# Performance work log

Measured on AMD Instinct MI355X. Metric: run time of the kernel, lower is better.

## Reference

```python
import jax, jax.numpy as jnp
import numpy as np

B, S, HID, NH, KCLIP = 2, 1500, 1024, 16, 64
HD = HID // NH  # 64


def setup_inputs() -> dict:
    key = jax.random.key(0)
    ks = jax.random.split(key, 16)
    std = 0.02
    inp = {
        "query": jax.random.normal(ks[0], (B, S, HID), jnp.float32),
        "key": jax.random.normal(ks[1], (B, S, HID), jnp.float32),
        "value": jax.random.normal(ks[2], (B, S, HID), jnp.float32),
        # per-head projection weights, stacked over heads: [NH, HID, HD]
        "Wq": jax.random.normal(ks[3], (NH, HID, HD), jnp.float32) * std,
        "bq": jax.random.normal(ks[4], (NH, HD), jnp.float32) * std,
        "Wk": jax.random.normal(ks[5], (NH, HID, HD), jnp.float32) * std,
        "bk": jax.random.normal(ks[6], (NH, HD), jnp.float32) * std,
        "Wv": jax.random.normal(ks[7], (NH, HID, HD), jnp.float32) * std,
        "bv": jax.random.normal(ks[8], (NH, HD), jnp.float32) * std,
        # Shaw relative-position embedding tables: [2k+1, HD]
        "pe_k": jax.random.normal(ks[9], (2 * KCLIP + 1, HD), jnp.float32) * std,
        "pe_v": jax.random.normal(ks[10], (2 * KCLIP + 1, HD), jnp.float32) * std,
        # output projection (torch Linear stored as x @ W + b here)
        "W_fc": jax.random.normal(ks[11], (HID, HID), jnp.float32) * std,
        "b_fc": jax.random.normal(ks[12], (HID,), jnp.float32) * std,
    }
    return inp


def _rel_bias(pe, length, k_clip):
    idx = jnp.arange(length)
    dist = jnp.clip(idx[None, :] - idx[:, None], -k_clip, k_clip) + k_clip
    return pe[dist]  # [S, S, HD]


def reference(query, key, value, Wq, bq, Wk, bk, Wv, bv, pe_k, pe_v, W_fc, b_fc):
    head_dim = Wq.shape[-1]
    seq = query.shape[1]
    k_clip = (pe_k.shape[0] - 1) // 2

    kb = _rel_bias(pe_k, seq, k_clip)  # [S, S, HD]
    vb = _rel_bias(pe_v, seq, k_clip)  # [S, S, HD]

    # batched per-head projections: [B, NH, S, HD]
    Q = jnp.einsum('bsh,nhd->bnsd', query, Wq) + bq[None, :, None, :]
    K = jnp.einsum('bsh,nhd->bnsd', key, Wk) + bk[None, :, None, :]
    V = jnp.einsum('bsh,nhd->bnsd', value, Wv) + bv[None, :, None, :]

    # content term + Shaw relative-key bias term
    scores = jnp.einsum('bnqd,bnkd->bnqk', Q, K) \
           + jnp.einsum('bnqd,qkd->bnqk', Q, kb)
    scores = scores / jnp.sqrt(jnp.asarray(head_dim, scores.dtype))

    w = jax.nn.softmax(scores, axis=-1)  # [B, NH, S, S]

    out = jnp.einsum('bnqk,bnkd->bnqd', w, V) \
        + jnp.einsum('bnqk,qkd->bnqd', w, vb)

    # concat heads (head order matches ModuleList concatenation)
    hidden = out.transpose(0, 2, 1, 3).reshape(query.shape[0], seq, -1)
    return hidden @ W_fc + b_fc
```

## Files before the change

kernel.cpp:

```cpp
#include <hip/hip_runtime.h>
#include <math.h>

#define B_     2
#define S_     1500
#define HID_   1024
#define NH_    16
#define HD_    64
#define M_     (B_*S_)
#define SP_    1536
#define LOG2E  1.4426950408889634f

typedef short bf16x8 __attribute__((ext_vector_type(8)));
typedef short bf16x4 __attribute__((ext_vector_type(4)));
typedef float f32x4  __attribute__((ext_vector_type(4)));

__device__ __forceinline__ float b2f(short s) {
    unsigned u = ((unsigned)(unsigned short)s) << 16;
    return __uint_as_float(u);
}
__device__ __forceinline__ short f2b(float f) {
    unsigned u = __float_as_uint(f);
    unsigned r = (u + 0x7FFFu + ((u >> 16) & 1u)) >> 16;
    return (short)r;
}
__device__ __forceinline__ void gload16(const short* src, short* lds) {
    __builtin_amdgcn_global_load_lds(
        (const __attribute__((address_space(1))) void*)src,
        (__attribute__((address_space(3))) void*)lds, 16, 0, 0);
}

__global__ __launch_bounds__(256) void cvt_act3(
    const float* __restrict__ q, const float* __restrict__ k,
    const float* __restrict__ v, short* __restrict__ oq,
    short* __restrict__ ok, short* __restrict__ ov)
{
    const float* src = blockIdx.y == 0 ? q : blockIdx.y == 1 ? k : v;
    short* dst       = blockIdx.y == 0 ? oq : blockIdx.y == 1 ? ok : ov;
    int i = blockIdx.x * 256 + threadIdx.x;
    const float4* p = (const float4*)(src + (size_t)i * 8);
    float4 a = p[0], b = p[1];
    bf16x8 o;
    o[0]=f2b(a.x); o[1]=f2b(a.y); o[2]=f2b(a.z); o[3]=f2b(a.w);
    o[4]=f2b(b.x); o[5]=f2b(b.y); o[6]=f2b(b.z); o[7]=f2b(b.w);
    *(bf16x8*)(dst + (size_t)i * 8) = o;
}

__global__ __launch_bounds__(256) void prep_w(
    const float* __restrict__ Wq, const float* __restrict__ Wk,
    const float* __restrict__ Wv, const float* __restrict__ Wfc,
    const float* __restrict__ pe_k, const float* __restrict__ pe_v,
    short* __restrict__ Wqt, short* __restrict__ Wkt, short* __restrict__ Wvt,
    short* __restrict__ Wfh, short* __restrict__ Wfl,
    short* __restrict__ pe_kb, short* __restrict__ pe_vt)
{
    int z = blockIdx.x, tid = threadIdx.x;
    if (z == 1024) {
        for (int s = tid; s < 144 * 64; s += 256) {
            int j = s >> 6, d = s & 63;
            pe_kb[s] = (j < 129) ? f2b(pe_k[j * 64 + d]) : (short)0;
        }
        for (int s = tid; s < 64 * 160; s += 256) {
            int d = s / 160, j = s - d * 160;
            pe_vt[s] = (j < 129) ? f2b(pe_v[j * 64 + d]) : (short)0;
        }
        return;
    }
    __shared__ float T[64][65];
    const float* src; short* dhi; short* dlo = nullptr;
    int C, c0, r0; float scale = 1.f;
    if (z < 768) {
        int widx = z >> 8, rem = z & 255;
        int h = rem >> 4, rt = rem & 15;
        src = (widx == 0 ? Wq : widx == 1 ? Wk : Wv) + (size_t)h * 1024 * 64;
        dhi = (widx == 0 ? Wqt : widx == 1 ? Wkt : Wvt) + (size_t)h * 64 * 1024;
        scale = (widx == 0) ? 0.125f * LOG2E : 1.0f;
        C = 64; c0 = 0; r0 = rt * 64;
    } else {
        int idx = z - 768;
        src = Wfc; dhi = Wfh; dlo = Wfl;
        C = 1024; c0 = (idx >> 4) * 64; r0 = (idx & 15) * 64;
    }
#pragma unroll
    for (int i = 0; i < 4; ++i) {
        int slot = tid + i * 256;
        int r = slot >> 4, cg = (slot & 15) * 4;
        float4 v = *(const float4*)(src + (size_t)(r0 + r) * C + c0 + cg);
        T[r][cg+0] = v.x*scale; T[r][cg+1] = v.y*scale;
        T[r][cg+2] = v.z*scale; T[r][cg+3] = v.w*scale;
    }
    __syncthreads();
#pragma unroll
    for (int i = 0; i < 16; ++i) {
        int slot = tid + i * 256;
        int c = slot >> 6, r = slot & 63;
        float v = T[r][c];
        short hi = f2b(v);
        size_t o = (size_t)(c0 + c) * 1024 + r0 + r;
        dhi[o] = hi;
        if (dlo) dlo[o] = f2b(v - b2f(hi));
    }
}

__device__ __forceinline__ void gemm_core(
    const short* __restrict__ Ahi, const short* __restrict__ Alo,
    const short* __restrict__ Bhi, const short* __restrict__ Blo,
    int kIters, int m0, int n0, short* As, short* Bs, f32x4 (&acc)[4][4])
{
    const int tid = threadIdx.x, w = tid >> 6, lane = tid & 63;
    const int l15 = lane & 15, lr4 = lane >> 4;
    const int wr = w >> 1, wc = w & 1;

    for (int it = 0; it < kIters; ++it) {
        int kt = it * 64;
        int seg = kt >> 10, kk0 = kt & 1023;
        const short* Aseg = (seg == 1) ? Alo : Ahi;
        const short* Bseg = (seg == 2) ? Blo : Bhi;
        __syncthreads();
#pragma unroll
        for (int c = 0; c < 4; ++c) {
            int slot = (w * 4 + c) * 64 + lane;
            int r = slot >> 3, cb = slot & 7;
            int sm = m0 + r; sm = sm < M_ ? sm : M_ - 1;
            gload16(Aseg + (size_t)sm * 1024 + kk0 + ((cb ^ (r & 7)) * 8),
                    As + (size_t)(w * 4 + c) * 512);
            gload16(Bseg + (size_t)(n0 + r) * 1024 + kk0 + ((cb ^ (r & 7)) * 8),
                    Bs + (size_t)(w * 4 + c) * 512);
        }
        __syncthreads();
#pragma unroll
        for (int kh = 0; kh < 2; ++kh) {
            bf16x8 aF[4], bF[4];
#pragma unroll
            for (int mi = 0; mi < 4; ++mi) {
                int r = wr * 64 + mi * 16 + l15;
                aF[mi] = *(const bf16x8*)(As + r * 64 + (((kh*4+lr4) ^ (r & 7)) * 8));
            }
#pragma unroll
            for (int ni = 0; ni < 4; ++ni) {
                int r = wc * 64 + ni * 16 + l15;
                bF[ni] = *(const bf16x8*)(Bs + r * 64 + (((kh*4+lr4) ^ (r & 7)) * 8));
            }
#pragma unroll
            for (int mi = 0; mi < 4; ++mi)
#pragma unroll
                for (int ni = 0; ni < 4; ++ni)
                    acc[mi][ni] = __builtin_amdgcn_mfma_f32_16x16x32_bf16(
                        aF[mi], bF[ni], acc[mi][ni], 0, 0, 0);
        }
    }
}

__global__ __launch_bounds__(256) void gemm_qkv(
    const short* __restrict__ qb, const short* __restrict__ kb,
    const short* __restrict__ vb, const short* __restrict__ Wqt,
    const short* __restrict__ Wkt, const short* __restrict__ Wvt,
    const float* __restrict__ bq, const float* __restrict__ bk,
    const float* __restrict__ bv,
    short* __restrict__ Qp, short* __restrict__ Kp, short* __restrict__ Vp)
{
    __shared__ short As[128 * 64];
    __shared__ short Bs[128 * 64];
    const int z = blockIdx.z;
    const short* A  = z == 0 ? qb : z == 1 ? kb : vb;
    const short* Bw = z == 0 ? Wqt : z == 1 ? Wkt : Wvt;
    const float* bias = z == 0 ? bq : z == 1 ? bk : bv;
    const float bscale = z == 0 ? 0.125f * LOG2E : 1.0f;
    short* out = z == 0 ? Qp : z == 1 ? Kp : Vp;
    const int m0 = blockIdx.x * 128, n0 = blockIdx.y * 128;

    f32x4 zf = {0.f,0.f,0.f,0.f};
    f32x4 acc[4][4];
#pragma unroll
    for (int i = 0; i < 4; ++i)
#pragma unroll
        for (int j = 0; j < 4; ++j) acc[i][j] = zf;

    gemm_core(A, A, Bw, Bw, 16, m0, n0, As, Bs, acc);

    const int tid = threadIdx.x, w = tid >> 6, lane = tid & 63;
    const int l15 = lane & 15, lr4 = lane >> 4;
    const int wr = w >> 1, wc = w & 1;
#pragma unroll
    for (int mi = 0; mi < 4; ++mi)
#pragma unroll
        for (int rr = 0; rr < 4; ++rr) {
            int m = m0 + wr * 64 + mi * 16 + lr4 * 4 + rr;
            if (m >= M_) continue;
            int b = m / S_, s = m - b * S_;
#pragma unroll
            for (int ni = 0; ni < 4; ++ni) {
                int n = n0 + wc * 64 + ni * 16 + l15;
                float v = acc[mi][ni][rr] + bias[n] * bscale;
                int h = n >> 6, d = n & 63;
                out[(((size_t)(b * NH_ + h)) * S_ + s) * HD_ + d] = f2b(v);
            }
        }
}

__global__ __launch_bounds__(256) void gemm_fc(
    const short* __restrict__ Ahi, const short* __restrict__ Alo,
    const short* __restrict__ Bhi, const short* __restrict__ Blo,
    const float* __restrict__ bias, float* __restrict__ out)
{
    __shared__ short As[128 * 64];
    __shared__ short Bs[128 * 64];
    const int m0 = blockIdx.x * 128, n0 = blockIdx.y * 128;
    f32x4 zf = {0.f,0.f,0.f,0.f};
    f32x4 acc[4][4];
#pragma unroll
    for (int i = 0; i < 4; ++i)
#pragma unroll
        for (int j = 0; j < 4; ++j) acc[i][j] = zf;

    gemm_core(Ahi, Alo, Bhi, Blo, 32, m0, n0, As, Bs, acc);

    const int tid = threadIdx.x, w = tid >> 6, lane = tid & 63;
    const int l15 = lane & 15, lr4 = lane >> 4;
    const int wr = w >> 1, wc = w & 1;
#pragma unroll
    for (int mi = 0; mi < 4; ++mi)
#pragma unroll
        for (int rr = 0; rr < 4; ++rr) {
            int m = m0 + wr * 64 + mi * 16 + lr4 * 4 + rr;
            if (m >= M_) continue;
#pragma unroll
            for (int ni = 0; ni < 4; ++ni) {
                int n = n0 + wc * 64 + ni * 16 + l15;
                out[(size_t)m * 1024 + n] = acc[mi][ni][rr] + bias[n];
            }
        }
}

__global__ __launch_bounds__(256) void vtrans(
    const short* __restrict__ Vp, short* __restrict__ Vtg)
{
    __shared__ short T[64][72];
    const int bh = blockIdx.y, s0 = blockIdx.x * 64, tid = threadIdx.x;
    const size_t kv = (size_t)bh * S_ * 64;
#pragma unroll
    for (int i = 0; i < 2; ++i) {
        int slot = tid + i * 256;
        int r = slot >> 3, cb = slot & 7;
        int ss = s0 + r; ss = ss < S_ ? ss : S_ - 1;
        bf16x8 v = *(const bf16x8*)(Vp + kv + (size_t)ss * 64 + cb * 8);
        *(bf16x8*)(&T[r][cb * 8]) = v;
    }
    __syncthreads();
#pragma unroll
    for (int i = 0; i < 2; ++i) {
        int slot = tid + i * 256;
        int d = slot >> 3, cg = slot & 7;
        bf16x8 v;
#pragma unroll
        for (int j = 0; j < 8; ++j) {
            int kk = 32 * (cg >> 2) + ((j >> 2) & 1) * 16 + (cg & 3) * 4 + (j & 3);
            v[j] = T[kk][d];
        }
        *(bf16x8*)(Vtg + ((size_t)bh * 64 + d) * SP_ + s0 + cg * 8) = v;
    }
}

__global__ __launch_bounds__(256) void attn_mfma(
    const short* __restrict__ Qb, const short* __restrict__ Kb,
    const short* __restrict__ Vtg, const short* __restrict__ pe_kb,
    const short* __restrict__ pe_vt,
    short* __restrict__ hid_hi, short* __restrict__ hid_lo)
{
    __shared__ short qpe[64 * 144];
    __shared__ short wsm[64 * 160];

    const int tid = threadIdx.x, w = tid >> 6, lane = tid & 63;
    const int l15 = lane & 15, lr4 = lane >> 4;
    const int lg = (blockIdx.x & 7) * 96 + (blockIdx.x >> 3);
    const int bh = lg / 24, bx = lg - bh * 24;
    const int q0 = bx * 64;
    const int qw = q0 + w * 16;
    const int myq = qw + l15;
    const int myrow = w * 16 + l15;
    const size_t kv  = (size_t)bh * S_ * HD_;
    const size_t vtb = (size_t)bh * 64 * SP_;

    {
        short ini = f2b(-1e30f);
        bf16x8 iv;
#pragma unroll
        for (int i = 0; i < 8; ++i) iv[i] = ini;
        short* base = wsm + w * 16 * 160;
#pragma unroll
        for (int i = 0; i < 5; ++i)
            *(bf16x8*)(base + (size_t)(i * 64 + lane) * 8) = iv;
    }

    bf16x8 qA[2];
    {
        int sq = myq < S_ ? myq : S_ - 1;
        const short* qp = Qb + kv + (size_t)sq * 64 + lr4 * 8;
        qA[0] = *(const bf16x8*)(qp);
        qA[1] = *(const bf16x8*)(qp + 32);
    }

    f32x4 zf = {0.f,0.f,0.f,0.f};
#pragma unroll
    for (int jt = 0; jt < 9; ++jt) {
        f32x4 a = zf;
#pragma unroll
        for (int kh = 0; kh < 2; ++kh) {
            bf16x8 pf = *(const bf16x8*)(pe_kb + (size_t)(jt * 16 + l15) * 64 + kh * 32 + lr4 * 8);
            a = __builtin_amdgcn_mfma_f32_16x16x32_bf16(pf, qA[kh], a, 0, 0, 0);
        }
        bf16x4 pk;
#pragma unroll
        for (int rr = 0; rr < 4; ++rr) pk[rr] = f2b(a[rr]);
        *(bf16x4*)(qpe + (size_t)myrow * 144 + jt * 16 + lr4 * 4) = pk;
    }
    const float qpe0   = b2f(qpe[myrow * 144 + 0]);
    const float qpe128 = b2f(qpe[myrow * 144 + 128]);

    float m = 0.f, s0s = 0.f, s1s = 0.f;
    f32x4 o[4];
#pragma unroll
    for (int t = 0; t < 4; ++t) o[t] = zf;

    for (int c = 0; c < 12; ++c) {
        const int kc = c * 128;

        const bool lo0 = (kc +  63 - qw) <= -64, hi0 = (kc       - (qw + 15)) >= 64;
        const bool lo1 = (kc + 127 - qw) <= -64, hi1 = (kc + 64  - (qw + 15)) >= 64;
        const bool mx0 = !(lo0 || hi0), mx1 = !(lo1 || hi1);
        const float ub0 = lo0 ? qpe0 : qpe128;
        const float ub1 = lo1 ? qpe0 : qpe128;

        bf16x8 kf[8][2];
#pragma unroll
        for (int t8 = 0; t8 < 8; ++t8) {
            int sk = kc + t8 * 16 + l15; sk = sk < S_ ? sk : S_ - 1;
            const short* kp = Kb + kv + (size_t)sk * 64 + lr4 * 8;
            kf[t8][0] = *(const bf16x8*)(kp);
            kf[t8][1] = *(const bf16x8*)(kp + 32);
        }

        float rm = -1e30f;
        bf16x8 pa[2][2];
#pragma unroll
        for (int t8 = 0; t8 < 8; ++t8) {
            f32x4 s = __builtin_amdgcn_mfma_f32_16x16x32_bf16(kf[t8][0], qA[0], zf, 0, 0, 0);
            s = __builtin_amdgcn_mfma_f32_16x16x32_bf16(kf[t8][1], qA[1], s, 0, 0, 0);

            const int h = t8 >> 2, tt = t8 & 3;
            const int wn = tt >> 1, sl = (tt & 1) * 4;
            const bool mx = h ? mx1 : mx0;
            const bool alo = h ? lo1 : lo0;
            const float ub = h ? ub1 : ub0;
#pragma unroll
            for (int rr = 0; rr < 4; ++rr) {
                int k = kc + t8 * 16 + lr4 * 4 + rr;
                int rel = k - myq;
                float v;
                if (mx) {
                    int jc = rel < -64 ? 0 : (rel > 64 ? 128 : rel + 64);
                    v = s[rr] + b2f(qpe[myrow * 144 + jc]);
                } else {
                    v = s[rr] + ub;
                }
                if (k >= S_) v = -1e30f;
                rm = fmaxf(rm, v);
                if (mx && rel > -64 && rel < 64)
                    wsm[myrow * 160 + rel + 64] = f2b(v);
                float p2 = exp2f(v - m);
                pa[h][wn][sl + rr] = f2b(p2);
                if (mx) {
                    if (rel <= -64) s0s += p2; else if (rel >= 64) s1s += p2;
                } else if (alo) s0s += p2; else s1s += p2;
            }
        }

        bf16x8 vf[16];
#pragma unroll
        for (int h = 0; h < 2; ++h)
#pragma unroll
            for (int wn = 0; wn < 2; ++wn)
#pragma unroll
                for (int td = 0; td < 4; ++td) {
                    int r = td * 16 + l15;
                    int cbv = h * 8 + wn * 4 + lr4;
                    vf[(h * 2 + wn) * 4 + td] = *(const bf16x8*)(
                        Vtg + vtb + (size_t)r * SP_ + kc + cbv * 8);
                }

        __builtin_amdgcn_s_setprio(1);
#pragma unroll
        for (int h = 0; h < 2; ++h)
#pragma unroll
            for (int wn = 0; wn < 2; ++wn)
#pragma unroll
                for (int td = 0; td < 4; ++td)
                    o[td] = __builtin_amdgcn_mfma_f32_16x16x32_bf16(
                        pa[h][wn], vf[(h * 2 + wn) * 4 + td], o[td], 0, 0, 0);
        __builtin_amdgcn_s_setprio(0);

        rm = fmaxf(rm, __shfl_xor(rm, 16));
        rm = fmaxf(rm, __shfl_xor(rm, 32));
        if (!__all(rm <= m + 8.f)) {
            float nm = fmaxf(m, rm);
            float fac = exp2f(m - nm);
            m = nm; s0s *= fac; s1s *= fac;
            float fo[4];
#pragma unroll
            for (int rr = 0; rr < 4; ++rr) fo[rr] = __shfl(fac, lr4 * 4 + rr);
#pragma unroll
            for (int t = 0; t < 4; ++t)
#pragma unroll
                for (int rr = 0; rr < 4; ++rr) o[t][rr] *= fo[rr];
        }
    }

    s0s += __shfl_xor(s0s, 16); s0s += __shfl_xor(s0s, 32);
    s1s += __shfl_xor(s1s, 16); s1s += __shfl_xor(s1s, 32);

    short* rowp = wsm + (size_t)myrow * 160;
    float midsum = 0.f;
#pragma unroll
    for (int cc = 0; cc < 5; ++cc) {
        int off = (cc * 4 + lr4) * 8;
        bf16x8 mv = *(const bf16x8*)(rowp + off);
        bf16x8 ev;
#pragma unroll
        for (int jj = 0; jj < 8; ++jj) {
            float e = exp2f(b2f(mv[jj]) - m);
            ev[jj] = f2b(e);
            midsum += e;
        }
        *(bf16x8*)(rowp + off) = ev;
    }
    midsum += __shfl_xor(midsum, 16); midsum += __shfl_xor(midsum, 32);
    const float linv = 1.f / (s0s + s1s + midsum);
    if (lr4 == 0) { rowp[0] = f2b(s0s); rowp[128] = f2b(s1s); }

#pragma unroll
    for (int jh = 0; jh < 5; ++jh) {
        bf16x8 aW = *(const bf16x8*)(wsm + (size_t)myrow * 160 + jh * 32 + lr4 * 8);
#pragma unroll
        for (int td = 0; td < 4; ++td) {
            bf16x8 bW = *(const bf16x8*)(pe_vt + (size_t)(td * 16 + l15) * 160 + jh * 32 + lr4 * 8);
            o[td] = __builtin_amdgcn_mfma_f32_16x16x32_bf16(aW, bW, o[td], 0, 0, 0);
        }
    }

    {
        float fo[4];
#pragma unroll
        for (int rr = 0; rr < 4; ++rr) fo[rr] = __shfl(linv, lr4 * 4 + rr);
#pragma unroll
        for (int td = 0; td < 4; ++td)
#pragma unroll
            for (int rr = 0; rr < 4; ++rr) o[td][rr] *= fo[rr];
    }

#pragma unroll
    for (int td = 0; td < 4; ++td)
#pragma unroll
        for (int rr = 0; rr < 4; ++rr) {
            int qrow = lr4 * 4 + rr;
            int d = td * 16 + l15;
            int inner = (((d >> 2) ^ ((qrow & 7) << 1)) << 2) + (d & 3);
            float v = o[td][rr];
            short hi = f2b(v);
            wsm[(w * 16 + qrow) * 160 + inner] = hi;
            qpe[(w * 16 + qrow) * 144 + inner] = f2b(v - b2f(hi));
        }
    {
        int b = bh >> 4, h = bh & 15;
        int qrow = lane >> 2;
        int q = q0 + w * 16 + qrow;
#pragma unroll
        for (int i = 0; i < 2; ++i) {
            int cb = (lane & 3) * 2 + i;
            int qws = (cb * 2) ^ ((qrow & 7) << 1);
            bf16x8 hv = *(const bf16x8*)(wsm + (w * 16 + qrow) * 160 + qws * 4);
            bf16x8 lv = *(const bf16x8*)(qpe + (w * 16 + qrow) * 144 + qws * 4);
            if (q < S_) {
                size_t oo = ((size_t)(b * S_ + q)) * 1024 + h * 64 + cb * 8;
                *(bf16x8*)(hid_hi + oo) = hv;
                *(bf16x8*)(hid_lo + oo) = lv;
            }
        }
    }
}

extern "C" void kernel_launch(void* const* d_in, const int* in_sizes, int n_in,
                              void* d_out, int out_size, void* d_ws, size_t ws_size,
                              hipStream_t stream)
{
    const float* query = (const float*)d_in[0];
    const float* key   = (const float*)d_in[1];
    const float* value = (const float*)d_in[2];
    const float* Wq    = (const float*)d_in[3];
    const float* bq    = (const float*)d_in[4];
    const float* Wk    = (const float*)d_in[5];
    const float* bk    = (const float*)d_in[6];
    const float* Wv    = (const float*)d_in[7];
    const float* bv    = (const float*)d_in[8];
    const float* pe_k  = (const float*)d_in[9];
    const float* pe_v  = (const float*)d_in[10];
    const float* W_fc  = (const float*)d_in[11];
    const float* b_fc  = (const float*)d_in[12];

    char* W = (char*)d_ws;
    short* qb   = (short*)(W + 0);
    short* kb   = (short*)(W + 6291456);
    short* vb   = (short*)(W + 12582912);
    short* Vtg  = vb;
    short* Wqt  = (short*)(W + 18874368);
    short* Wkt  = (short*)(W + 20971520);
    short* Wvt  = (short*)(W + 23068672);
    short* Wfh  = (short*)(W + 25165824);
    short* Wfl  = (short*)(W + 27262976);
    short* Qp   = (short*)(W + 29360128);
    short* Kp   = (short*)(W + 35651584);
    short* Vp   = (short*)(W + 41943040);
    short* pekb = (short*)(W + 48234496);
    short* pevt = (short*)(W + 48252928);
    short* hidh = qb;
    short* hidl = kb;

    cvt_act3<<<dim3(1500, 3), 256, 0, stream>>>(query, key, value, qb, kb, vb);
    prep_w<<<1025, 256, 0, stream>>>(Wq, Wk, Wv, W_fc, pe_k, pe_v,
                                     Wqt, Wkt, Wvt, Wfh, Wfl, pekb, pevt);
    gemm_qkv<<<dim3(24, 8, 3), 256, 0, stream>>>(qb, kb, vb, Wqt, Wkt, Wvt,
                                                 bq, bk, bv, Qp, Kp, Vp);
    vtrans<<<dim3(24, 32), 256, 0, stream>>>(Vp, Vtg);
    attn_mfma<<<768, 256, 0, stream>>>(Qp, Kp, Vtg, pekb, pevt, hidh, hidl);
    gemm_fc<<<dim3(24, 8), 256, 0, stream>>>(hidh, hidl, Wfh, Wfl, b_fc, (float*)d_out);
}
```

Measured before the change: 283.2 us.

## Split attention key range across wave pairs and merge partial softmax in LDS

Each attention block now handles 32 queries instead of 64. The four waves are arranged as two query sub-tiles times two halves of the key range, and the grid roughly doubles to 1504 blocks. Each wave runs 6 key chunks instead of 12. The second-half waves write their running max, partial sums and output accumulators to shared memory, and the first-half waves rescale and merge them before finishing the relative-position band and the output store. The aim is more parallelism and shorter per-wave serial loops. The cost is an extra block-wide sync, extra LDS traffic for the merge, and Q/positional-bias setup now repeated per key half.

```diff
diff --git a/kernel.cpp b/kernel.cpp
--- a/kernel.cpp
+++ b/kernel.cpp
@@ -9,6 +9,7 @@
 #define M_     (B_*S_)
 #define SP_    1536
 #define LOG2E  1.4426950408889634f
+#define QB_    47
 
 typedef short bf16x8 __attribute__((ext_vector_type(8)));
 typedef short bf16x4 __attribute__((ext_vector_type(4)));
@@ -266,26 +267,31 @@
     const short* __restrict__ pe_vt,
     short* __restrict__ hid_hi, short* __restrict__ hid_lo)
 {
-    __shared__ short qpe[64 * 144];
-    __shared__ short wsm[64 * 160];
+    __shared__ short qpe[32 * 144];
+    __shared__ short wsm[32 * 160];
+    __shared__ float comb_o[2][16][64];
+    __shared__ float comb_s0[2][16];
+    __shared__ float comb_s1[2][16];
+    __shared__ float comb_m[2];
 
     const int tid = threadIdx.x, w = tid >> 6, lane = tid & 63;
     const int l15 = lane & 15, lr4 = lane >> 4;
-    const int lg = (blockIdx.x & 7) * 96 + (blockIdx.x >> 3);
-    const int bh = lg / 24, bx = lg - bh * 24;
-    const int q0 = bx * 64;
-    const int qw = q0 + w * 16;
+    const int qsub = w >> 1, khalf = w & 1;
+    const int lg = (blockIdx.x & 7) * 188 + (blockIdx.x >> 3);
+    const int bh = lg / QB_, bx = lg - bh * QB_;
+    const int q0 = bx * 32;
+    const int qw = q0 + qsub * 16;
     const int myq = qw + l15;
-    const int myrow = w * 16 + l15;
+    const int myrow = qsub * 16 + l15;
     const size_t kv  = (size_t)bh * S_ * HD_;
     const size_t vtb = (size_t)bh * 64 * SP_;
 
-    {
+    if (khalf == 0) {
         short ini = f2b(-1e30f);
         bf16x8 iv;
 #pragma unroll
         for (int i = 0; i < 8; ++i) iv[i] = ini;
-        short* base = wsm + w * 16 * 160;
+        short* base = wsm + qsub * 16 * 160;
 #pragma unroll
         for (int i = 0; i < 5; ++i)
             *(bf16x8*)(base + (size_t)(i * 64 + lane) * 8) = iv;
@@ -313,6 +319,8 @@
         for (int rr = 0; rr < 4; ++rr) pk[rr] = f2b(a[rr]);
         *(bf16x4*)(qpe + (size_t)myrow * 144 + jt * 16 + lr4 * 4) = pk;
     }
+    __syncthreads();
+
     const float qpe0   = b2f(qpe[myrow * 144 + 0]);
     const float qpe128 = b2f(qpe[myrow * 144 + 128]);
 
@@ -321,8 +329,8 @@
 #pragma unroll
     for (int t = 0; t < 4; ++t) o[t] = zf;
 
-    for (int c = 0; c < 12; ++c) {
-        const int kc = c * 128;
+    for (int c = 0; c < 6; ++c) {
+        const int kc = khalf * 768 + c * 128;
 
         const bool lo0 = (kc +  63 - qw) <= -64, hi0 = (kc       - (qw + 15)) >= 64;
         const bool lo1 = (kc + 127 - qw) <= -64, hi1 = (kc + 64  - (qw + 15)) >= 64;
@@ -417,6 +425,33 @@
     s0s += __shfl_xor(s0s, 16); s0s += __shfl_xor(s0s, 32);
     s1s += __shfl_xor(s1s, 16); s1s += __shfl_xor(s1s, 32);
 
+    if (khalf == 1) {
+        if (lane == 0) comb_m[qsub] = m;
+        if (lr4 == 0) { comb_s0[qsub][l15] = s0s; comb_s1[qsub][l15] = s1s; }
+#pragma unroll
+        for (int td = 0; td < 4; ++td)
+#pragma unroll
+            for (int rr = 0; rr < 4; ++rr)
+                comb_o[qsub][lr4 * 4 + rr][td * 16 + l15] = o[td][rr];
+    }
+    __syncthreads();
+    if (khalf == 1) return;
+
+    {
+        float mo = comb_m[qsub];
+        float M = fmaxf(m, mo);
+        float fs = exp2f(m - M), ft = exp2f(mo - M);
+#pragma unroll
+        for (int td = 0; td < 4; ++td)
+#pragma unroll
+            for (int rr = 0; rr < 4; ++rr)
+                o[td][rr] = o[td][rr] * fs
+                          + comb_o[qsub][lr4 * 4 + rr][td * 16 + l15] * ft;
+        s0s = s0s * fs + comb_s0[qsub][l15] * ft;
+        s1s = s1s * fs + comb_s1[qsub][l15] * ft;
+        m = M;
+    }
+
     short* rowp = wsm + (size_t)myrow * 160;
     float midsum = 0.f;
 #pragma unroll
@@ -465,19 +500,19 @@
             int inner = (((d >> 2) ^ ((qrow & 7) << 1)) << 2) + (d & 3);
             float v = o[td][rr];
             short hi = f2b(v);
-            wsm[(w * 16 + qrow) * 160 + inner] = hi;
-            qpe[(w * 16 + qrow) * 144 + inner] = f2b(v - b2f(hi));
+            wsm[(qsub * 16 + qrow) * 160 + inner] = hi;
+            qpe[(qsub * 16 + qrow) * 144 + inner] = f2b(v - b2f(hi));
         }
     {
         int b = bh >> 4, h = bh & 15;
         int qrow = lane >> 2;
-        int q = q0 + w * 16 + qrow;
+        int q = q0 + qsub * 16 + qrow;
 #pragma unroll
         for (int i = 0; i < 2; ++i) {
             int cb = (lane & 3) * 2 + i;
             int qws = (cb * 2) ^ ((qrow & 7) << 1);
-            bf16x8 hv = *(const bf16x8*)(wsm + (w * 16 + qrow) * 160 + qws * 4);
-            bf16x8 lv = *(const bf16x8*)(qpe + (w * 16 + qrow) * 144 + qws * 4);
+            bf16x8 hv = *(const bf16x8*)(wsm + (qsub * 16 + qrow) * 160 + qws * 4);
+            bf16x8 lv = *(const bf16x8*)(qpe + (qsub * 16 + qrow) * 144 + qws * 4);
             if (q < S_) {
                 size_t oo = ((size_t)(b * S_ + q)) * 1024 + h * 64 + cb * 8;
                 *(bf16x8*)(hid_hi + oo) = hv;
@@ -529,6 +564,6 @@
     gemm_qkv<<<dim3(24, 8, 3), 256, 0, stream>>>(qb, kb, vb, Wqt, Wkt, Wvt,
                                                  bq, bk, bv, Qp, Kp, Vp);
     vtrans<<<dim3(24, 32), 256, 0, stream>>>(Vp, Vtg);
-    attn_mfma<<<768, 256, 0, stream>>>(Qp, Kp, Vtg, pekb, pevt, hidh, hidl);
+    attn_mfma<<<8 * 188, 256, 0, stream>>>(Qp, Kp, Vtg, pekb, pevt, hidh, hidl);
     gemm_fc<<<dim3(24, 8), 256, 0, stream>>>(hidh, hidl, Wfh, Wfl, b_fc, (float*)d_out);
 }
```

Result: no change. 285.2 us (+0.7%).
